# Kernel optimization log

Measured on AMD Instinct MI355X. Metric: run time of the kernel, lower is better.

The kernel has to match this reference:

```python
import jax, jax.numpy as jnp
import numpy as np

B, T, F, H, V = 4096, 128, 256, 64, 32
EMB = 8
IN = EMB + 1  # 8-dim feature embedding + 1 Y_past channel
EPS = 1e-3    # keras LayerNorm/BatchNorm default epsilon


def lstm(x, Wk, Wr, b, h0, c0):
    """Keras-convention LSTM (gate order i,f,g,o). x: [B,T,D] -> ([B,T,H], h, c)."""
    def step(carry, xt):
        h, c = carry
        z = xt @ Wk + h @ Wr + b
        i, f, g, o = jnp.split(z, 4, axis=-1)
        c = jax.nn.sigmoid(f) * c + jax.nn.sigmoid(i) * jnp.tanh(g)
        h = jax.nn.sigmoid(o) * jnp.tanh(c)
        return (h, c), h
    (h, c), hs = jax.lax.scan(step, (h0, c0), jnp.swapaxes(x, 0, 1))
    return jnp.swapaxes(hs, 0, 1), h, c


def setup_inputs() -> dict:
    key = jax.random.key(0)
    ks = iter(jax.random.split(key, 32))
    n = lambda *s: jax.random.normal(next(ks), s, jnp.float32) * 0.05
    return {
        "X": jax.random.normal(next(ks), (B, T, F), jnp.float32),
        "Y_past": jax.random.randint(next(ks), (B, T), 0, V),
        "ln_gamma": jnp.ones((F,), jnp.float32), "ln_beta": jnp.zeros((F,), jnp.float32),
        "W1": n(F, 32), "b1": jnp.zeros((32,), jnp.float32),
        "bn_gamma": jnp.ones((32,), jnp.float32), "bn_beta": jnp.zeros((32,), jnp.float32),
        "bn_mean": jnp.zeros((32,), jnp.float32), "bn_var": jnp.ones((32,), jnp.float32),
        "W2": n(32, 16), "b2": jnp.zeros((16,), jnp.float32),
        "W3": n(16, EMB), "b3": jnp.zeros((EMB,), jnp.float32),
        "enc_fk": n(IN, 4 * H), "enc_fr": n(H, 4 * H), "enc_fb": jnp.zeros((4 * H,), jnp.float32),
        "enc_bk": n(IN, 4 * H), "enc_br": n(H, 4 * H), "enc_bb": jnp.zeros((4 * H,), jnp.float32),
        "Wsh": n(2 * H, H), "bsh": jnp.zeros((H,), jnp.float32),
        "Wsc": n(2 * H, H), "bsc": jnp.zeros((H,), jnp.float32),
        "Wq": n(H, 2 * H), "bq": jnp.zeros((2 * H,), jnp.float32),
        "dec_k": n(2 * H, 4 * H), "dec_r": n(H, 4 * H), "dec_b": jnp.zeros((4 * H,), jnp.float32),
        "Wo": n(H, V), "bo": jnp.zeros((V,), jnp.float32),
    }


def reference(X, Y_past, ln_gamma, ln_beta, W1, b1, bn_gamma, bn_beta, bn_mean, bn_var,
              W2, b2, W3, b3, enc_fk, enc_fr, enc_fb, enc_bk, enc_br, enc_bb,
              Wsh, bsh, Wsc, bsc, Wq, bq, dec_k, dec_r, dec_b, Wo, bo):
    b = X.shape[0]
    # LayerNorm over feature axis
    mu = jnp.mean(X, axis=-1, keepdims=True)
    var = jnp.var(X, axis=-1, keepdims=True)
    xn = (X - mu) * jax.lax.rsqrt(var + EPS) * ln_gamma + ln_beta
    # feature MLP (dropout inactive at inference); BatchNorm in inference mode
    e = jax.nn.relu(xn @ W1 + b1)
    e = (e - bn_mean) * jax.lax.rsqrt(bn_var + EPS) * bn_gamma + bn_beta
    e = jax.nn.relu(e @ W2 + b2)
    e = jax.nn.relu(e @ W3 + b3)
    seq = jnp.concatenate([e, Y_past.astype(jnp.float32)[..., None]], axis=-1)  # [B,T,9]
    # Bidirectional LSTM encoder (merge_mode='concat')
    h0 = jnp.zeros((b, H), seq.dtype)
    c0 = jnp.zeros((b, H), seq.dtype)
    fwd_out, fh, fc = lstm(seq, enc_fk, enc_fr, enc_fb, h0, c0)
    bwd_out, bh, bc = lstm(seq[:, ::-1], enc_bk, enc_br, enc_bb, h0, c0)
    enc = jnp.concatenate([fwd_out, bwd_out[:, ::-1]], axis=-1)  # [B,T,2H]
    # state projections and query
    sh = jnp.concatenate([fh, bh], axis=-1) @ Wsh + bsh  # [B,H]
    sc = jnp.concatenate([fc, bc], axis=-1) @ Wsc + bsc  # [B,H]
    q = (sh @ Wq + bq)[:, None, :]                       # [B,1,2H]
    # keras Attention: dot-product scores, softmax over keys
    scores = jnp.einsum('bqd,btd->bqt', q, enc)
    w = jax.nn.softmax(scores, axis=-1)
    att = jnp.einsum('bqt,btd->bqd', w, enc)             # [B,1,2H]
    # decoder LSTM (length-1 sequence) with projected initial state
    dec_out, _, _ = lstm(att, dec_k, dec_r, dec_b, sh, sc)  # [B,1,H]
    return jax.nn.softmax(dec_out @ Wo + bo, axis=-1)       # [B,1,V]
```

## Files before the change

kernel.cpp:

```cpp
#include <hip/hip_runtime.h>
#include <math.h>

#define BB 4096
#define TT 128
#define FF 256
#define VV 32
#define LN_EPS 1e-3f

typedef __attribute__((ext_vector_type(8))) short short8;
typedef __attribute__((ext_vector_type(4))) float f32x4;

template <int M> struct IC { static constexpr int value = M; };

__device__ __forceinline__ float sigm(float x) {
    return __builtin_amdgcn_rcpf(1.0f + __builtin_amdgcn_exp2f(-1.442695041f * x));
}
__device__ __forceinline__ float tanhfast(float x) {
    float e = __builtin_amdgcn_exp2f(2.885390082f * x);
    return 1.0f - 2.0f * __builtin_amdgcn_rcpf(e + 1.0f);
}
__device__ __forceinline__ unsigned short f2bf(float f) {
    union { float f; unsigned u; } v; v.f = f;
    unsigned r = v.u + 0x7FFFu + ((v.u >> 16) & 1u);
    return (unsigned short)(r >> 16);
}
__device__ __forceinline__ float bf2f(unsigned short h) {
    union { unsigned u; float f; } v; v.u = ((unsigned)h) << 16; return v.f;
}

__global__ __launch_bounds__(256, 3) void k_mlp2(
    const float* __restrict__ X, const int* __restrict__ Yp,
    const float* __restrict__ lng, const float* __restrict__ lnb,
    const float* __restrict__ W1, const float* __restrict__ b1,
    const float* __restrict__ bng, const float* __restrict__ bnb,
    const float* __restrict__ bnm, const float* __restrict__ bnv,
    const float* __restrict__ W2, const float* __restrict__ b2,
    const float* __restrict__ W3, const float* __restrict__ b3,
    unsigned int* __restrict__ sqpk, unsigned short* __restrict__ yv)
{
    __shared__ unsigned short w1fh[8192], w1fl[8192];
    __shared__ unsigned short w2fh[512], w2fl[512];
    __shared__ unsigned short w3fh[512], w3fl[512];
    __shared__ float bD1[32], bnSs[32], bnBs[32], b2s[16], b3s[8];
    __shared__ float e1s[4][16][33];
    __shared__ float e2s[4][16][17];

    const int tid = threadIdx.x;
    for (int e = tid; e < 8192; e += 256) {
        int j = e & 7, lane = (e >> 3) & 63, nt = (e >> 9) & 1, ks = e >> 10;
        int c = ks * 32 + (lane >> 4) * 8 + j;
        int n = nt * 16 + (lane & 15);
        float v = lng[c] * W1[c * 32 + n];
        unsigned short hi = f2bf(v);
        w1fh[e] = hi; w1fl[e] = f2bf(v - bf2f(hi));
    }
    for (int e = tid; e < 512; e += 256) {
        int j = e & 7, lane = e >> 3;
        int k = (lane >> 4) * 8 + j, n = lane & 15;
        float v2 = W2[k * 16 + n];
        unsigned short h2 = f2bf(v2);
        w2fh[e] = h2; w2fl[e] = f2bf(v2 - bf2f(h2));
        float v3 = (k < 16 && n < 8) ? W3[k * 8 + n] : 0.f;
        unsigned short h3 = f2bf(v3);
        w3fh[e] = h3; w3fl[e] = f2bf(v3 - bf2f(h3));
    }
    if (tid < 32) {
        float a = b1[tid];
        for (int c2 = 0; c2 < 256; ++c2) a += lnb[c2] * W1[c2 * 32 + tid];
        bD1[tid] = a;
        float sc = bng[tid] * rsqrtf(bnv[tid] + LN_EPS);
        bnSs[tid] = sc; bnBs[tid] = bnb[tid] - bnm[tid] * sc;
    } else if (tid < 48) b2s[tid - 32] = b2[tid - 32];
    else if (tid < 56) b3s[tid - 48] = b3[tid - 48];
    __syncthreads();

    const int wv = tid >> 6, l = tid & 63;
    const int r = l & 15, q = l >> 4;
    const int ntiles = (BB * TT) / 16;
    for (int tile = blockIdx.x * 4 + wv; tile < ntiles; tile += gridDim.x * 4) {
        const size_t rowbase = (size_t)tile * 16;
        const float* xrow = X + (rowbase + r) * FF + q * 8;
        float xd[64];
        #pragma unroll
        for (int ks = 0; ks < 8; ++ks) {
            float4 p0 = *(const float4*)(xrow + ks * 32);
            float4 p1 = *(const float4*)(xrow + ks * 32 + 4);
            xd[ks * 8 + 0] = p0.x; xd[ks * 8 + 1] = p0.y; xd[ks * 8 + 2] = p0.z; xd[ks * 8 + 3] = p0.w;
            xd[ks * 8 + 4] = p1.x; xd[ks * 8 + 5] = p1.y; xd[ks * 8 + 6] = p1.z; xd[ks * 8 + 7] = p1.w;
        }
        float s = 0.f, ss = 0.f;
        #pragma unroll
        for (int i = 0; i < 64; ++i) { s += xd[i]; ss += xd[i] * xd[i]; }
        s += __shfl_xor(s, 16);  s += __shfl_xor(s, 32);
        ss += __shfl_xor(ss, 16); ss += __shfl_xor(ss, 32);
        float mu = s * (1.0f / FF);
        float var = ss * (1.0f / FF) - mu * mu;
        float rs = rsqrtf(var + LN_EPS);

        f32x4 acc0 = {bD1[r], bD1[r], bD1[r], bD1[r]};
        f32x4 acc1 = {bD1[16 + r], bD1[16 + r], bD1[16 + r], bD1[16 + r]};
        #pragma unroll
        for (int ks = 0; ks < 8; ++ks) {
            short8 ah, al;
            #pragma unroll
            for (int j = 0; j < 8; ++j) {
                float xn = (xd[ks * 8 + j] - mu) * rs;
                unsigned short hi = f2bf(xn);
                ah[j] = (short)hi; al[j] = (short)f2bf(xn - bf2f(hi));
            }
            short8 bh0 = *(const short8*)&w1fh[((ks * 2 + 0) * 64 + l) * 8];
            short8 bl0 = *(const short8*)&w1fl[((ks * 2 + 0) * 64 + l) * 8];
            short8 bh1 = *(const short8*)&w1fh[((ks * 2 + 1) * 64 + l) * 8];
            short8 bl1 = *(const short8*)&w1fl[((ks * 2 + 1) * 64 + l) * 8];
            acc0 = __builtin_amdgcn_mfma_f32_16x16x32_bf16(ah, bh0, acc0, 0, 0, 0);
            acc0 = __builtin_amdgcn_mfma_f32_16x16x32_bf16(al, bh0, acc0, 0, 0, 0);
            acc0 = __builtin_amdgcn_mfma_f32_16x16x32_bf16(ah, bl0, acc0, 0, 0, 0);
            acc1 = __builtin_amdgcn_mfma_f32_16x16x32_bf16(ah, bh1, acc1, 0, 0, 0);
            acc1 = __builtin_amdgcn_mfma_f32_16x16x32_bf16(al, bh1, acc1, 0, 0, 0);
            acc1 = __builtin_amdgcn_mfma_f32_16x16x32_bf16(ah, bl1, acc1, 0, 0, 0);
        }
        #pragma unroll
        for (int i = 0; i < 4; ++i) {
            int row = q * 4 + i;
            float z0 = fmaxf(acc0[i], 0.f) * bnSs[r] + bnBs[r];
            float z1 = fmaxf(acc1[i], 0.f) * bnSs[16 + r] + bnBs[16 + r];
            e1s[wv][row][r] = z0;
            e1s[wv][row][16 + r] = z1;
        }
        __builtin_amdgcn_wave_barrier();

        short8 a2h, a2l;
        #pragma unroll
        for (int j = 0; j < 8; ++j) {
            float v = e1s[wv][r][q * 8 + j];
            unsigned short hi = f2bf(v);
            a2h[j] = (short)hi; a2l[j] = (short)f2bf(v - bf2f(hi));
        }
        f32x4 acc2 = {b2s[r], b2s[r], b2s[r], b2s[r]};
        {
            short8 bh = *(const short8*)&w2fh[l * 8];
            short8 bl = *(const short8*)&w2fl[l * 8];
            acc2 = __builtin_amdgcn_mfma_f32_16x16x32_bf16(a2h, bh, acc2, 0, 0, 0);
            acc2 = __builtin_amdgcn_mfma_f32_16x16x32_bf16(a2l, bh, acc2, 0, 0, 0);
            acc2 = __builtin_amdgcn_mfma_f32_16x16x32_bf16(a2h, bl, acc2, 0, 0, 0);
        }
        #pragma unroll
        for (int i = 0; i < 4; ++i) e2s[wv][q * 4 + i][r] = fmaxf(acc2[i], 0.f);
        __builtin_amdgcn_wave_barrier();

        short8 a3h = (short8){0,0,0,0,0,0,0,0}, a3l = (short8){0,0,0,0,0,0,0,0};
        if (q < 2) {
            #pragma unroll
            for (int j = 0; j < 8; ++j) {
                float v = e2s[wv][r][q * 8 + j];
                unsigned short hi = f2bf(v);
                a3h[j] = (short)hi; a3l[j] = (short)f2bf(v - bf2f(hi));
            }
        }
        float b3v = (r < 8) ? b3s[r] : 0.f;
        f32x4 acc3 = {b3v, b3v, b3v, b3v};
        {
            short8 bh = *(const short8*)&w3fh[l * 8];
            short8 bl = *(const short8*)&w3fl[l * 8];
            acc3 = __builtin_amdgcn_mfma_f32_16x16x32_bf16(a3h, bh, acc3, 0, 0, 0);
            acc3 = __builtin_amdgcn_mfma_f32_16x16x32_bf16(a3l, bh, acc3, 0, 0, 0);
            acc3 = __builtin_amdgcn_mfma_f32_16x16x32_bf16(a3h, bl, acc3, 0, 0, 0);
        }
        if (r < 8) {
            #pragma unroll
            for (int i = 0; i < 4; ++i) {
                size_t grow = rowbase + q * 4 + i;
                float e3 = fmaxf(acc3[i], 0.f);
                unsigned int wself = (unsigned)f2bf(e3);
                unsigned int wnbr = __shfl_xor(wself, 1);
                if ((r & 1) == 0) sqpk[grow * 4 + (r >> 1)] = (wnbr << 16) | wself;
            }
        } else if (r == 8) {
            #pragma unroll
            for (int i = 0; i < 4; ++i) {
                size_t grow = rowbase + q * 4 + i;
                yv[grow] = f2bf((float)Yp[grow]);
            }
        }
        __builtin_amdgcn_wave_barrier();
    }
}

#define R1_SEQ 0u
#define R1_YV  34816u
#define R1_HP  38912u
#define R1_SZ  48128u

__global__ __launch_bounds__(512, 1) void k_rnn1(
    const unsigned int* __restrict__ g_sqpk, const unsigned short* __restrict__ g_yv,
    const float* __restrict__ fk, const float* __restrict__ fr, const float* __restrict__ fb,
    const float* __restrict__ bk, const float* __restrict__ br, const float* __restrict__ bbv,
    unsigned int* __restrict__ enc,
    float* __restrict__ hfin, float* __restrict__ cfin,
    int s0)
{
    __shared__ __align__(16) unsigned char arena[R1_SZ];
    unsigned int*   seqU   = (unsigned int*)(arena + R1_SEQ);
    unsigned short* yvS    = (unsigned short*)(arena + R1_YV);
    unsigned int*   hpackU = (unsigned int*)(arena + R1_HP);

    const int tid = threadIdx.x;
    const int sbase = s0 + blockIdx.x * 16;
    const int wv = tid >> 6, l = tid & 63;
    const int d = wv >> 2, w = wv & 3;
    const int r = l & 15, q = l >> 4;
    const int u = (w << 4) + r;

    for (int i = tid; i < 16 * TT * 4; i += 512) {
        int smp = i >> 9, rem = i & 511;
        int t = rem >> 2, j = rem & 3;
        seqU[t * 68 + smp * 4 + j] = g_sqpk[(size_t)(sbase + smp) * (TT * 4) + rem];
    }
    for (int i = tid; i < 16 * TT; i += 512) {
        int smp = i >> 7, t = i & 127;
        yvS[t * 16 + smp] = g_yv[(size_t)(sbase + smp) * TT + t];
    }

    const float* Wr = d ? br : fr;
    const float* Wk = d ? bk : fk;
    const float* Bz = d ? bbv : fb;
    short8 Bh[3][4];
    float bz[4];
    #pragma unroll
    for (int g = 0; g < 4; ++g) {
        int col = (g << 6) + u;
        bz[g] = Bz[col];
        #pragma unroll
        for (int kt = 0; kt < 3; ++kt) {
            #pragma unroll
            for (int j = 0; j < 8; ++j) {
                int kg = kt * 32 + q * 8 + j;
                float v = (kg < 64) ? Wr[kg * 256 + col]
                        : (kg < 73) ? Wk[(kg - 64) * 256 + col] : 0.f;
                Bh[kt][g][j] = (short)f2bf(v);
            }
        }
    }

    const unsigned int* hrd0 = hpackU + (d * 16 + r) * 36 + q * 4;
    const unsigned int* hrd1 = hrd0 + 1152;
    const int wofs = w * 8 + (r >> 1);
    const int elb = ((blockIdx.x * 16 + q * 4) * TT) * 64 + d * 32 + (u >> 1);

    for (int i = tid; i < 2304; i += 512) hpackU[i] = 0u;
    float c4[4] = {0.f, 0.f, 0.f, 0.f};
    __syncthreads();

    auto ldA2 = [&](int ts_) -> short8 {
        short8 v = (short8){0,0,0,0,0,0,0,0};
        if (q == 0)      v = *(const short8*)(seqU + ts_ * 68 + r * 4);
        else if (q == 1) v[0] = (short)yvS[ts_ * 16 + r];
        return v;
    };
    short8 A2h = ldA2(d ? (TT - 1) : 0);

    for (int t = 0; t < TT; ++t) {
        const int ts = d ? (TT - 1 - t) : t;
        const int buf = t & 1;
        const unsigned int* hp = buf ? hrd1 : hrd0;
        short8 A0h = *(const short8*)(hp);
        short8 A1h = *(const short8*)(hp + 16);
        short8 A2c = A2h;

        f32x4 z[4];
        #pragma unroll
        for (int g = 0; g < 4; ++g) {
            f32x4 acc = {bz[g], bz[g], bz[g], bz[g]};
            acc = __builtin_amdgcn_mfma_f32_16x16x32_bf16(A0h, Bh[0][g], acc, 0, 0, 0);
            acc = __builtin_amdgcn_mfma_f32_16x16x32_bf16(A1h, Bh[1][g], acc, 0, 0, 0);
            acc = __builtin_amdgcn_mfma_f32_16x16x32_bf16(A2c, Bh[2][g], acc, 0, 0, 0);
            z[g] = acc;
        }

        if (t < TT - 1) A2h = ldA2(d ? (TT - 2 - t) : (t + 1));

        const int nbase = ((buf ^ 1) * 2 + d) * 16;
        #pragma unroll
        for (int i = 0; i < 4; ++i) {
            float zi = z[0][i], zf = z[1][i], zg = z[2][i], zo = z[3][i];
            float cc = sigm(zf) * c4[i] + sigm(zi) * tanhfast(zg);
            float hh = sigm(zo) * tanhfast(cc);
            c4[i] = cc;
            int smp = (q << 2) + i;
            unsigned int wself = (unsigned)f2bf(hh);
            unsigned int wnbr = __shfl_xor(wself, 1);
            if ((r & 1) == 0) {
                unsigned int outw = (wnbr << 16) | wself;
                hpackU[(nbase + smp) * 36 + wofs] = outw;
                enc[elb + i * (TT * 64) + ts * 64] = outw;
            }
            if (t == TT - 1) {
                hfin[(size_t)(sbase + smp) * 128 + (d << 6) + u] = hh;
                cfin[(size_t)(sbase + smp) * 128 + (d << 6) + u] = cc;
            }
        }
        asm volatile("s_waitcnt lgkmcnt(0)\n\ts_barrier" ::: "memory");
    }
}

__global__ __launch_bounds__(256, 4) void k_att(
    const unsigned short* __restrict__ enc,
    const float* __restrict__ hfin, const float* __restrict__ cfin,
    const float* __restrict__ Wsh, const float* __restrict__ bsh,
    const float* __restrict__ Wsc, const float* __restrict__ bsc,
    const float* __restrict__ Wq,  const float* __restrict__ bq,
    const float* __restrict__ dk,  const float* __restrict__ dr, const float* __restrict__ dbv,
    const float* __restrict__ Wo,  const float* __restrict__ bo,
    float* __restrict__ out, int s0)
{
    __shared__ unsigned short el[TT][136];
    __shared__ float st[128], ct[128], shS[64], scS[64], qS[128], pS[128], attS[128], zdS[256], hdS[64], red[8];

    int tid = threadIdx.x;
    int bloc = blockIdx.x;
    int s = s0 + bloc;

    for (int i = tid; i < TT * 16; i += 256) {
        int t = i >> 4, c = i & 15;
        *(short8*)&el[t][c * 8] = *(const short8*)&enc[(size_t)bloc * TT * 128 + t * 128 + c * 8];
    }
    if (tid < 128) { st[tid] = hfin[(size_t)s * 128 + tid]; ct[tid] = cfin[(size_t)s * 128 + tid]; }
    __syncthreads();

    if (tid < 128) {
        int uu = tid & 63;
        const float* Wm = (tid < 64) ? Wsh : Wsc;
        const float* sv = (tid < 64) ? st : ct;
        float a = (tid < 64) ? bsh[uu] : bsc[uu];
        #pragma unroll 4
        for (int j = 0; j < 128; ++j) a += sv[j] * Wm[j * 64 + uu];
        if (tid < 64) shS[uu] = a; else scS[uu] = a;
    }
    __syncthreads();
    if (tid < 128) {
        float a = bq[tid];
        #pragma unroll 4
        for (int uu = 0; uu < 64; ++uu) a += shS[uu] * Wq[uu * 128 + tid];
        qS[tid] = a;
    }
    __syncthreads();
    float sc_val = 0.f;
    int wvv = tid >> 6, lnn = tid & 63;
    if (tid < 128) {
        float a = 0.f;
        #pragma unroll 2
        for (int c = 0; c < 16; ++c) {
            short8 e8 = *(const short8*)&el[tid][c * 8];
            #pragma unroll
            for (int j2 = 0; j2 < 8; ++j2) a += qS[c * 8 + j2] * bf2f((unsigned short)e8[j2]);
        }
        sc_val = a;
        float m = a;
        #pragma unroll
        for (int mk = 1; mk < 64; mk <<= 1) m = fmaxf(m, __shfl_xor(m, mk));
        if (lnn == 0) red[wvv] = m;
    }
    __syncthreads();
    float gmax = fmaxf(red[0], red[1]);
    if (tid < 128) {
        float ev = expf(sc_val - gmax);
        pS[tid] = ev;
        float s2 = ev;
        #pragma unroll
        for (int mk = 1; mk < 64; mk <<= 1) s2 += __shfl_xor(s2, mk);
        if (lnn == 0) red[4 + wvv] = s2;
    }
    __syncthreads();
    float denom = red[4] + red[5];
    if (tid < 128) {
        float a = 0.f;
        #pragma unroll 4
        for (int t2 = 0; t2 < TT; ++t2) a += pS[t2] * bf2f(el[t2][tid]);
        attS[tid] = a / denom;
    }
    __syncthreads();
    if (tid < 256) {
        float a = dbv[tid];
        #pragma unroll 4
        for (int j = 0; j < 128; ++j) a += attS[j] * dk[j * 256 + tid];
        #pragma unroll 4
        for (int j = 0; j < 64; ++j)  a += shS[j] * dr[j * 256 + tid];
        zdS[tid] = a;
    }
    __syncthreads();
    if (tid < 64) {
        float zi = zdS[tid], zf = zdS[64 + tid], zg = zdS[128 + tid], zo = zdS[192 + tid];
        float cc = sigm(zf) * scS[tid] + sigm(zi) * tanhfast(zg);
        hdS[tid] = sigm(zo) * tanhfast(cc);
    }
    __syncthreads();
    if (tid < 32) {
        float a = bo[tid];
        #pragma unroll
        for (int uu = 0; uu < 64; ++uu) a += hdS[uu] * Wo[uu * 32 + tid];
        float m = a;
        #pragma unroll
        for (int mk = 1; mk < 32; mk <<= 1) m = fmaxf(m, __shfl_xor(m, mk));
        float e = expf(a - m);
        float s2 = e;
        #pragma unroll
        for (int mk = 1; mk < 32; mk <<= 1) s2 += __shfl_xor(s2, mk);
        out[(size_t)s * VV + tid] = e / s2;
    }
}

#define A_SEQ   0u
#define A_YV    34816u
#define A_HP    38912u
#define A_SGRID 56320u
#define A_SH    72704u
#define A_SC    76800u
#define A_Q     80896u
#define A_ATT   89088u
#define A_L     97280u
#define A_SZ    97344u

__global__ __launch_bounds__(512, 1) void k_rnn(
    const unsigned int* __restrict__ g_sqpk, const unsigned short* __restrict__ g_yv,
    const float* __restrict__ fk, const float* __restrict__ fr, const float* __restrict__ fb,
    const float* __restrict__ bk, const float* __restrict__ br, const float* __restrict__ bbv,
    const float* __restrict__ Wsh, const float* __restrict__ bsh,
    const float* __restrict__ Wsc, const float* __restrict__ bsc,
    const float* __restrict__ Wq,  const float* __restrict__ bq,
    const float* __restrict__ dk,  const float* __restrict__ dr, const float* __restrict__ db,
    const float* __restrict__ Wo,  const float* __restrict__ bo,
    float* __restrict__ out)
{
    __shared__ __align__(16) unsigned char arena[A_SZ];
    unsigned int*   seqU   = (unsigned int*)(arena + A_SEQ);
    unsigned short* yvS    = (unsigned short*)(arena + A_YV);
    unsigned int*   hpackU = (unsigned int*)(arena + A_HP);
    float* sgridF = (float*)(arena + A_SGRID);
    float* hfinL  = (float*)(arena + A_SGRID);
    float* cfinL  = hfinL + 2048;
    float* zdS    = (float*)(arena + A_SGRID);
    float* shS    = (float*)(arena + A_SH);
    float* scS    = (float*)(arena + A_SC);
    float* qS     = (float*)(arena + A_Q);
    float* pT     = (float*)(arena + A_Q);
    float* attS   = (float*)(arena + A_ATT);
    float* hdS    = (float*)(arena + A_ATT);
    float* lS     = (float*)(arena + A_L);

    const int tid = threadIdx.x;
    const int sbase = blockIdx.x * 16;
    const int wv = tid >> 6, l = tid & 63;
    const int d = wv >> 2, w = wv & 3;
    const int r = l & 15, q = l >> 4;
    const int u = (w << 4) + r;

    for (int i = tid; i < 16 * TT * 4; i += 512) {
        int smp = i >> 9, rem = i & 511;
        int t = rem >> 2, j = rem & 3;
        seqU[t * 68 + smp * 4 + j] = g_sqpk[(size_t)(sbase + smp) * (TT * 4) + rem];
    }
    for (int i = tid; i < 16 * TT; i += 512) {
        int smp = i >> 7, t = i & 127;
        yvS[t * 16 + smp] = g_yv[(size_t)(sbase + smp) * TT + t];
    }

    const float* Wr = d ? br : fr;
    const float* Wk = d ? bk : fk;
    const float* Bz = d ? bbv : fb;
    short8 Bh[3][4], Bl[3][4];
    float bz[4];
    #pragma unroll
    for (int g = 0; g < 4; ++g) {
        int col = (g << 6) + u;
        bz[g] = Bz[col];
        #pragma unroll
        for (int kt = 0; kt < 3; ++kt) {
            #pragma unroll
            for (int j = 0; j < 8; ++j) {
                int kg = kt * 32 + q * 8 + j;
                float v = (kg < 64) ? Wr[kg * 256 + col]
                        : (kg < 73) ? Wk[(kg - 64) * 256 + col] : 0.f;
                unsigned short hi = f2bf(v);
                Bh[kt][g][j] = (short)hi;
                Bl[kt][g][j] = (short)f2bf(v - bf2f(hi));
            }
        }
    }
    short8 Bq0h = (short8){0,0,0,0,0,0,0,0}, Bq1h = (short8){0,0,0,0,0,0,0,0};

    const unsigned int* hrd0 = hpackU + (d * 16 + r) * 68 + q * 4;
    const unsigned int* hrd1 = hrd0 + 2176;
    const int wofs = w * 8 + (r >> 1) + ((r & 1) ? 32 : 0);
    __syncthreads();

    auto run_phase = [&](auto mode_c) {
        constexpr int mode = decltype(mode_c)::value;
        for (int i = tid; i < 4352; i += 512) hpackU[i] = 0u;
        float c4[4] = {0.f, 0.f, 0.f, 0.f};
        float aacc[4] = {0.f, 0.f, 0.f, 0.f};
        __syncthreads();
        for (int t = 0; t < TT; ++t) {
            const int ts = d ? (TT - 1 - t) : t;
            const int buf = t & 1;
            const unsigned int* hp = buf ? hrd1 : hrd0;
            short8 A0h = *(const short8*)(hp);
            short8 A1h = *(const short8*)(hp + 16);
            short8 A0l = *(const short8*)(hp + 32);
            short8 A1l = *(const short8*)(hp + 48);
            short8 A2h = (short8){0,0,0,0,0,0,0,0};
            if (q == 0) {
                A2h = *(const short8*)(seqU + ts * 68 + r * 4);
            } else if (q == 1) {
                A2h[0] = (short)yvS[ts * 16 + r];
            }
            if constexpr (mode == 1) {
                if (w == 0 && t > 0) {
                    f32x4 sa = {0.f, 0.f, 0.f, 0.f};
                    sa = __builtin_amdgcn_mfma_f32_16x16x32_bf16(A0h, Bq0h, sa, 0, 0, 0);
                    sa = __builtin_amdgcn_mfma_f32_16x16x32_bf16(A1h, Bq1h, sa, 0, 0, 0);
                    if (q == (r >> 2)) {
                        int tp = d ? (TT - t) : (t - 1);
                        sgridF[(d * 16 + r) * 128 + tp] = sa[r & 3];
                    }
                }
            }
            f32x4 z[4];
            #pragma unroll
            for (int g = 0; g < 4; ++g) {
                f32x4 acc = {bz[g], bz[g], bz[g], bz[g]};
                acc = __builtin_amdgcn_mfma_f32_16x16x32_bf16(A0h, Bh[0][g], acc, 0, 0, 0);
                acc = __builtin_amdgcn_mfma_f32_16x16x32_bf16(A0l, Bh[0][g], acc, 0, 0, 0);
                acc = __builtin_amdgcn_mfma_f32_16x16x32_bf16(A0h, Bl[0][g], acc, 0, 0, 0);
                acc = __builtin_amdgcn_mfma_f32_16x16x32_bf16(A1h, Bh[1][g], acc, 0, 0, 0);
                acc = __builtin_amdgcn_mfma_f32_16x16x32_bf16(A1l, Bh[1][g], acc, 0, 0, 0);
                acc = __builtin_amdgcn_mfma_f32_16x16x32_bf16(A1h, Bl[1][g], acc, 0, 0, 0);
                acc = __builtin_amdgcn_mfma_f32_16x16x32_bf16(A2h, Bh[2][g], acc, 0, 0, 0);
                acc = __builtin_amdgcn_mfma_f32_16x16x32_bf16(A2h, Bl[2][g], acc, 0, 0, 0);
                z[g] = acc;
            }
            const int nbase = ((buf ^ 1) * 2 + d) * 16;
            #pragma unroll
            for (int i = 0; i < 4; ++i) {
                float zi = z[0][i], zf = z[1][i], zg = z[2][i], zo = z[3][i];
                float cc = sigm(zf) * c4[i] + sigm(zi) * tanhfast(zg);
                float hh = sigm(zo) * tanhfast(cc);
                c4[i] = cc;
                int smp = (q << 2) + i;
                unsigned short bfh = f2bf(hh);
                unsigned short bfe = f2bf(hh - bf2f(bfh));
                unsigned int wself = ((unsigned)bfh << 16) | (unsigned)bfe;
                unsigned int wnbr = __shfl_xor(wself, 1);
                unsigned int outw = (r & 1) ? ((wself << 16) | (wnbr & 0xFFFFu))
                                            : ((wnbr & 0xFFFF0000u) | (wself >> 16));
                hpackU[(nbase + smp) * 68 + wofs] = outw;
                if constexpr (mode == 2) aacc[i] += pT[ts * 16 + smp] * hh;
                if constexpr (mode == 0) {
                    if (t == TT - 1) {
                        hfinL[smp * 128 + (d << 6) + u] = hh;
                        cfinL[smp * 128 + (d << 6) + u] = cc;
                    }
                }
            }
            __syncthreads();
        }
        if constexpr (mode == 1) {
            if (w == 0) {
                short8 A0h = *(const short8*)(hrd0);
                short8 A1h = *(const short8*)(hrd0 + 16);
                f32x4 sa = {0.f, 0.f, 0.f, 0.f};
                sa = __builtin_amdgcn_mfma_f32_16x16x32_bf16(A0h, Bq0h, sa, 0, 0, 0);
                sa = __builtin_amdgcn_mfma_f32_16x16x32_bf16(A1h, Bq1h, sa, 0, 0, 0);
                if (q == (r >> 2)) {
                    int tp = d ? 0 : (TT - 1);
                    sgridF[(d * 16 + r) * 128 + tp] = sa[r & 3];
                }
            }
            __syncthreads();
        }
        if constexpr (mode == 2) {
            #pragma unroll
            for (int i = 0; i < 4; ++i) {
                int smp = (q << 2) + i;
                attS[smp * 128 + (d << 6) + u] = aacc[i] / lS[smp];
            }
            __syncthreads();
        }
    };

    run_phase(IC<0>{});
    for (int o = tid; o < 2048; o += 512) {
        int kind = o >> 10, smp = (o >> 6) & 15, uu = o & 63;
        const float* src = kind ? (cfinL + smp * 128) : (hfinL + smp * 128);
        const float* Wm = kind ? Wsc : Wsh;
        float a = kind ? bsc[uu] : bsh[uu];
        #pragma unroll 4
        for (int j = 0; j < 128; ++j) a += src[j] * Wm[j * 64 + uu];
        (kind ? scS : shS)[smp * 64 + uu] = a;
    }
    __syncthreads();
    for (int o = tid; o < 2048; o += 512) {
        int smp = o >> 7, dd = o & 127;
        float a = bq[dd];
        #pragma unroll 4
        for (int j = 0; j < 64; ++j) a += shS[smp * 64 + j] * Wq[j * 128 + dd];
        qS[smp * 128 + dd] = a;
    }
    __syncthreads();
    if (w == 0) {
        #pragma unroll
        for (int j = 0; j < 8; ++j) {
            Bq0h[j] = (short)f2bf(qS[r * 128 + (d << 6) + q * 8 + j]);
            Bq1h[j] = (short)f2bf(qS[r * 128 + (d << 6) + 32 + q * 8 + j]);
        }
    }
    __syncthreads();

    run_phase(IC<1>{});
    {
        int smp = tid >> 5, sl = tid & 31;
        float sv[4];
        #pragma unroll
        for (int p = 0; p < 4; ++p) {
            int t = sl + 32 * p;
            sv[p] = sgridF[smp * 128 + t] + sgridF[(16 + smp) * 128 + t];
        }
        float m = fmaxf(fmaxf(sv[0], sv[1]), fmaxf(sv[2], sv[3]));
        #pragma unroll
        for (int mk = 1; mk < 32; mk <<= 1) m = fmaxf(m, __shfl_xor(m, mk));
        float lsum = 0.f;
        #pragma unroll
        for (int p = 0; p < 4; ++p) lsum += __expf(sv[p] - m);
        #pragma unroll
        for (int mk = 1; mk < 32; mk <<= 1) lsum += __shfl_xor(lsum, mk);
        __syncthreads();
        #pragma unroll
        for (int p = 0; p < 4; ++p) pT[(sl + 32 * p) * 16 + smp] = __expf(sv[p] - m);
        if (sl == 0) lS[smp] = lsum;
    }
    __syncthreads();

    run_phase(IC<2>{});

    for (int o = tid; o < 4096; o += 512) {
        int smp = o >> 8, col = o & 255;
        float a = db[col];
        #pragma unroll 4
        for (int j = 0; j < 128; ++j) a += attS[smp * 128 + j] * dk[j * 256 + col];
        #pragma unroll 4
        for (int j = 0; j < 64; ++j)  a += shS[smp * 64 + j] * dr[j * 256 + col];
        zdS[smp * 256 + col] = a;
    }
    __syncthreads();
    for (int o = tid; o < 1024; o += 512) {
        int smp = o >> 6, uu = o & 63;
        float zi = zdS[smp * 256 + uu], zf = zdS[smp * 256 + 64 + uu];
        float zg = zdS[smp * 256 + 128 + uu], zo = zdS[smp * 256 + 192 + uu];
        float cc = sigm(zf) * scS[smp * 64 + uu] + sigm(zi) * tanhfast(zg);
        hdS[smp * 64 + uu] = sigm(zo) * tanhfast(cc);
    }
    __syncthreads();
    {
        int smp = tid >> 5, v = tid & 31;
        float a = bo[v];
        #pragma unroll 4
        for (int j = 0; j < 64; ++j) a += hdS[smp * 64 + j] * Wo[j * 32 + v];
        float m = a;
        #pragma unroll
        for (int mk = 1; mk < 32; mk <<= 1) m = fmaxf(m, __shfl_xor(m, mk));
        float e = __expf(a - m);
        float s2 = e;
        #pragma unroll
        for (int mk = 1; mk < 32; mk <<= 1) s2 += __shfl_xor(s2, mk);
        out[(size_t)(sbase + smp) * VV + v] = e / s2;
    }
}

extern "C" void kernel_launch(void* const* d_in, const int* in_sizes, int n_in,
                              void* d_out, int out_size, void* d_ws, size_t ws_size,
                              hipStream_t stream) {
    const float* X   = (const float*)d_in[0];
    const int*   Yp  = (const int*)d_in[1];
    const float* lng = (const float*)d_in[2];
    const float* lnb = (const float*)d_in[3];
    const float* W1  = (const float*)d_in[4];
    const float* b1  = (const float*)d_in[5];
    const float* bng = (const float*)d_in[6];
    const float* bnb = (const float*)d_in[7];
    const float* bnm = (const float*)d_in[8];
    const float* bnv = (const float*)d_in[9];
    const float* W2  = (const float*)d_in[10];
    const float* b2  = (const float*)d_in[11];
    const float* W3  = (const float*)d_in[12];
    const float* b3  = (const float*)d_in[13];
    const float* fk  = (const float*)d_in[14];
    const float* fr  = (const float*)d_in[15];
    const float* fb  = (const float*)d_in[16];
    const float* bk  = (const float*)d_in[17];
    const float* br  = (const float*)d_in[18];
    const float* bbv = (const float*)d_in[19];
    const float* Wsh = (const float*)d_in[20];
    const float* bsh = (const float*)d_in[21];
    const float* Wsc = (const float*)d_in[22];
    const float* bsc = (const float*)d_in[23];
    const float* Wq  = (const float*)d_in[24];
    const float* bq  = (const float*)d_in[25];
    const float* dk  = (const float*)d_in[26];
    const float* dr  = (const float*)d_in[27];
    const float* db  = (const float*)d_in[28];
    const float* Wo  = (const float*)d_in[29];
    const float* bo  = (const float*)d_in[30];

    unsigned int*   sqpk = (unsigned int*)d_ws;
    unsigned short* yv   = (unsigned short*)(sqpk + (size_t)BB * TT * 4);
    float*          hfin = (float*)(yv + (size_t)BB * TT);
    float*          cfin = hfin + (size_t)BB * 128;
    unsigned int*   encp = (unsigned int*)(cfin + (size_t)BB * 128);
    const size_t baseB = (size_t)((char*)encp - (char*)d_ws);
    const size_t encFull = (size_t)BB * TT * 128 * 2;

    int nch = 0;
    if      (ws_size >= baseB + encFull)     nch = 1;
    else if (ws_size >= baseB + encFull / 2) nch = 2;
    else if (ws_size >= baseB + encFull / 4) nch = 4;
    else if (ws_size >= baseB + encFull / 8) nch = 8;

    k_mlp2<<<768, 256, 0, stream>>>(X, Yp, lng, lnb, W1, b1, bng, bnb, bnm, bnv,
                                    W2, b2, W3, b3, sqpk, yv);
    if (nch) {
        const int cs = BB / nch;
        for (int c = 0; c < nch; ++c) {
            int s0 = c * cs;
            k_rnn1<<<cs / 16, 512, 0, stream>>>(sqpk, yv, fk, fr, fb, bk, br, bbv,
                                                encp, hfin, cfin, s0);
            k_att<<<cs, 256, 0, stream>>>((const unsigned short*)encp, hfin, cfin,
                                          Wsh, bsh, Wsc, bsc, Wq, bq,
                                          dk, dr, db, Wo, bo, (float*)d_out, s0);
        }
    } else {
        k_rnn<<<BB / 16, 512, 0, stream>>>(sqpk, yv, fk, fr, fb, bk, br, bbv,
                                           Wsh, bsh, Wsc, bsc, Wq, bq, dk, dr, db, Wo, bo,
                                           (float*)d_out);
    }
}
```

Before: 426.2 us.

## Split BiLSTM encoder blocks by direction with eight samples per block

The encoder recurrence kernel now uses one 256-thread block per direction per 8-sample group, instead of a 512-thread block that handled both directions for 16 samples. Only half of each MFMA row tile carries live samples, so half the MFMA work is padding. In exchange the grid has four times as many blocks and each block needs less shared memory, which should give more latency hiding across the serial 128-step chain. The cost is that weight registers are loaded and the sequence staged into LDS by more blocks.

```diff
diff --git a/kernel.cpp b/kernel.cpp
--- a/kernel.cpp
+++ b/kernel.cpp
@@ -186,12 +186,12 @@
     }
 }
 
-#define R1_SEQ 0u
-#define R1_YV  34816u
-#define R1_HP  38912u
-#define R1_SZ  48128u
-
-__global__ __launch_bounds__(512, 1) void k_rnn1(
+#define R2_SEQ 0u
+#define R2_YV  18432u
+#define R2_HP  20480u
+#define R2_SZ  25088u
+
+__global__ __launch_bounds__(256, 2) void k_rnn2(
     const unsigned int* __restrict__ g_sqpk, const unsigned short* __restrict__ g_yv,
     const float* __restrict__ fk, const float* __restrict__ fr, const float* __restrict__ fb,
     const float* __restrict__ bk, const float* __restrict__ br, const float* __restrict__ bbv,
@@ -199,26 +199,30 @@
     float* __restrict__ hfin, float* __restrict__ cfin,
     int s0)
 {
-    __shared__ __align__(16) unsigned char arena[R1_SZ];
-    unsigned int*   seqU   = (unsigned int*)(arena + R1_SEQ);
-    unsigned short* yvS    = (unsigned short*)(arena + R1_YV);
-    unsigned int*   hpackU = (unsigned int*)(arena + R1_HP);
+    __shared__ __align__(16) unsigned char arena[R2_SZ];
+    unsigned int*   seqU   = (unsigned int*)(arena + R2_SEQ);
+    unsigned short* yvS    = (unsigned short*)(arena + R2_YV);
+    unsigned int*   hpackU = (unsigned int*)(arena + R2_HP);
 
     const int tid = threadIdx.x;
-    const int sbase = s0 + blockIdx.x * 16;
-    const int wv = tid >> 6, l = tid & 63;
-    const int d = wv >> 2, w = wv & 3;
+    const int grp = blockIdx.x >> 1;
+    const int d = blockIdx.x & 1;
+    const int sbase = s0 + grp * 8;
+    const int w = tid >> 6, l = tid & 63;
     const int r = l & 15, q = l >> 4;
     const int u = (w << 4) + r;
-
-    for (int i = tid; i < 16 * TT * 4; i += 512) {
+    const int rb = r & 3;
+    const int live = (rb < 2);
+    const int sloc = (r >> 2) * 2 + rb;
+
+    for (int i = tid; i < 8 * TT * 4; i += 256) {
         int smp = i >> 9, rem = i & 511;
         int t = rem >> 2, j = rem & 3;
-        seqU[t * 68 + smp * 4 + j] = g_sqpk[(size_t)(sbase + smp) * (TT * 4) + rem];
-    }
-    for (int i = tid; i < 16 * TT; i += 512) {
+        seqU[t * 36 + smp * 4 + j] = g_sqpk[(size_t)(sbase + smp) * (TT * 4) + rem];
+    }
+    for (int i = tid; i < 8 * TT; i += 256) {
         int smp = i >> 7, t = i & 127;
-        yvS[t * 16 + smp] = g_yv[(size_t)(sbase + smp) * TT + t];
+        yvS[t * 8 + smp] = g_yv[(size_t)(sbase + smp) * TT + t];
     }
 
     const float* Wr = d ? br : fr;
@@ -242,19 +246,22 @@
         }
     }
 
-    const unsigned int* hrd0 = hpackU + (d * 16 + r) * 36 + q * 4;
-    const unsigned int* hrd1 = hrd0 + 1152;
+    const unsigned int* hrd0 = hpackU + r * 36 + q * 4;
+    const unsigned int* hrd1 = hrd0 + 576;
     const int wofs = w * 8 + (r >> 1);
-    const int elb = ((blockIdx.x * 16 + q * 4) * TT) * 64 + d * 32 + (u >> 1);
-
-    for (int i = tid; i < 2304; i += 512) hpackU[i] = 0u;
-    float c4[4] = {0.f, 0.f, 0.f, 0.f};
+    const int elb = ((grp * 8 + q * 2) * TT) * 64 + d * 32 + (u >> 1);
+
+    for (int i = tid; i < 1152; i += 256) hpackU[i] = 0u;
+    float c4[2] = {0.f, 0.f};
     __syncthreads();
 
     auto ldA2 = [&](int ts_) -> short8 {
         short8 v = (short8){0,0,0,0,0,0,0,0};
-        if (q == 0)      v = *(const short8*)(seqU + ts_ * 68 + r * 4);
-        else if (q == 1) v[0] = (short)yvS[ts_ * 16 + r];
+        if (q == 0) {
+            if (live) v = *(const short8*)(seqU + ts_ * 36 + sloc * 4);
+        } else if (q == 1) {
+            if (live) v[0] = (short)yvS[ts_ * 8 + sloc];
+        }
         return v;
     };
     short8 A2h = ldA2(d ? (TT - 1) : 0);
@@ -279,24 +286,23 @@
 
         if (t < TT - 1) A2h = ldA2(d ? (TT - 2 - t) : (t + 1));
 
-        const int nbase = ((buf ^ 1) * 2 + d) * 16;
-        #pragma unroll
-        for (int i = 0; i < 4; ++i) {
+        const int nb = (buf ^ 1) * 576;
+        #pragma unroll
+        for (int i = 0; i < 2; ++i) {
             float zi = z[0][i], zf = z[1][i], zg = z[2][i], zo = z[3][i];
             float cc = sigm(zf) * c4[i] + sigm(zi) * tanhfast(zg);
             float hh = sigm(zo) * tanhfast(cc);
             c4[i] = cc;
-            int smp = (q << 2) + i;
             unsigned int wself = (unsigned)f2bf(hh);
             unsigned int wnbr = __shfl_xor(wself, 1);
             if ((r & 1) == 0) {
                 unsigned int outw = (wnbr << 16) | wself;
-                hpackU[(nbase + smp) * 36 + wofs] = outw;
+                hpackU[nb + (q * 4 + i) * 36 + wofs] = outw;
                 enc[elb + i * (TT * 64) + ts * 64] = outw;
             }
             if (t == TT - 1) {
-                hfin[(size_t)(sbase + smp) * 128 + (d << 6) + u] = hh;
-                cfin[(size_t)(sbase + smp) * 128 + (d << 6) + u] = cc;
+                hfin[(size_t)(sbase + q * 2 + i) * 128 + (d << 6) + u] = hh;
+                cfin[(size_t)(sbase + q * 2 + i) * 128 + (d << 6) + u] = cc;
             }
         }
         asm volatile("s_waitcnt lgkmcnt(0)\n\ts_barrier" ::: "memory");
@@ -730,8 +736,8 @@
         const int cs = BB / nch;
         for (int c = 0; c < nch; ++c) {
             int s0 = c * cs;
-            k_rnn1<<<cs / 16, 512, 0, stream>>>(sqpk, yv, fk, fr, fb, bk, br, bbv,
-                                                encp, hfin, cfin, s0);
+            k_rnn2<<<cs / 4, 256, 0, stream>>>(sqpk, yv, fk, fr, fb, bk, br, bbv,
+                                               encp, hfin, cfin, s0);
             k_att<<<cs, 256, 0, stream>>>((const unsigned short*)encp, hfin, cfin,
                                           Wsh, bsh, Wsc, bsc, Wq, bq,
                                           dk, dr, db, Wo, bo, (float*)d_out, s0);
```

Result: slower. 448.7 us (+5.3%).
